# Kernel optimization log

Measured on AMD Instinct MI355X. Metric: run time of the kernel, lower is better.

Reference implementation:

```python
import jax, jax.numpy as jnp
import numpy as np

H = 8          # num_heads
DM = 128       # dmodel
BN_EPS = 1e-5


def _linear(x, w, b):
    # w stored as [in, out]
    return x @ w + b


def _relu_mha(q, k, v, qw, qb, kw, kb, vw, vb, ow, ob, mask):
    """TemMulHeadAtte: ReLU on projected Q/K/V, masked softmax, ReLU out-proj.
    q,k: [B,N,T,2*DM]; v: [B,N,T,DM]; mask: broadcastable to [B,N,H,T,T] or None."""
    B, N, T, _ = q.shape
    Q = jax.nn.relu(_linear(q, qw, qb)).reshape(B, N, T, H, -1)  # e = 2*DM/H
    K = jax.nn.relu(_linear(k, kw, kb)).reshape(B, N, T, H, -1)
    V = jax.nn.relu(_linear(v, vw, vb)).reshape(B, N, T, H, -1)  # d = DM/H
    scale = 1.0 / np.sqrt(Q.shape[-1]).astype(np.float32)
    scores = jnp.einsum('bnthe,bnshe->bnhts', Q, K)
    if mask is not None:
        scores = jnp.where(mask, -jnp.inf, scores)
    attn = jax.nn.softmax(scale * scores, axis=-1)  # dropout p=0 -> identity
    out = jnp.einsum('bnhts,bnshd->bnthd', attn, V).reshape(B, N, T, -1)
    return jax.nn.relu(_linear(out, ow, ob))


def setup_inputs() -> dict:
    key = jax.random.key(0)
    ks = iter(jax.random.split(key, 32))
    B, N, T = 16, 207, 24
    def w(shape, scale=0.05):
        return (jax.random.normal(next(ks), shape, dtype=jnp.float32) * scale)
    inp = {
        'x': w((B, N, T, DM), 1.0),
        'hidden': w((B, N, T, DM), 1.0),
        'tXin': w((B, N, T, DM), 1.0),
    }
    dk = 2 * DM // H * H   # 256
    dv = DM // H * H       # 128
    for pre in ('s', 't'):  # space / temporal attention params
        inp[pre + 'q_w'] = w((2 * DM, dk)); inp[pre + 'q_b'] = w((dk,))
        inp[pre + 'k_w'] = w((2 * DM, dk)); inp[pre + 'k_b'] = w((dk,))
        inp[pre + 'v_w'] = w((DM, dv));     inp[pre + 'v_b'] = w((dv,))
        inp[pre + 'o_w'] = w((dv, DM));     inp[pre + 'o_b'] = w((DM,))
    inp['gate_w'] = w((2 * DM, DM)); inp['gate_b'] = w((DM,))
    inp['bn_gamma'] = jnp.ones((DM,), jnp.float32)
    inp['bn_beta'] = jnp.zeros((DM,), jnp.float32)
    return inp


def reference(x, hidden, tXin,
              sq_w, sq_b, sk_w, sk_b, sv_w, sv_b, so_w, so_b,
              tq_w, tq_b, tk_w, tk_b, tv_w, tv_b, to_w, to_b,
              gate_w, gate_b, bn_gamma, bn_beta):
    B, N, T, E = hidden.shape
    ht = jnp.concatenate([hidden, tXin], axis=3)  # [B,N,T,2*DM]
    # spatial attention: attend over nodes (N<->T permute)
    sqk = ht.transpose(0, 2, 1, 3)        # [B,T,N,2*DM]
    sval = hidden.transpose(0, 2, 1, 3)   # [B,T,N,DM]
    spaceOut = _relu_mha(sqk, sqk, sval, sq_w, sq_b, sk_w, sk_b, sv_w, sv_b,
                         so_w, so_b, None).transpose(0, 2, 1, 3)  # [B,N,T,DM]
    # temporal attention with causal (strict upper-tri) mask
    mask = jnp.triu(jnp.ones((T, T), dtype=bool), 1)[None, None, None]
    tempOut = _relu_mha(ht, ht, hidden, tq_w, tq_b, tk_w, tk_b, tv_w, tv_b,
                        to_w, to_b, mask)  # [B,N,T,DM]
    # gate + BatchNorm2d over channel dim (training-mode batch stats, biased var)
    gi = _linear(jnp.concatenate([spaceOut, tempOut], axis=3), gate_w, gate_b)
    mean = gi.mean(axis=(0, 1, 2))
    var = gi.var(axis=(0, 1, 2))
    z = jax.nn.sigmoid((gi - mean) * jax.lax.rsqrt(var + BN_EPS) * bn_gamma + bn_beta)
    return z * spaceOut + (1.0 - z) * tempOut
```

## Files before the change

kernel.cpp:

```cpp
#include <hip/hip_runtime.h>
#include <hip/hip_bf16.h>

typedef __bf16 bf16;
typedef __bf16 bf16x2 __attribute__((ext_vector_type(2)));
typedef __bf16 bf16x8 __attribute__((ext_vector_type(8)));
typedef float f32x4 __attribute__((ext_vector_type(4)));

#define MTOT 79488
#define NDIM 207
#define TDIM 24

#define EXP2F(x) __builtin_amdgcn_exp2f(x)

__global__ void detect_dtype(const void* __restrict__ hidden, int* __restrict__ flag,
                             float* __restrict__ stats)
{
    __shared__ int cnt;
    if (threadIdx.x == 0) cnt = 0;
    stats[threadIdx.x] = 0.f;
    __syncthreads();
    const bf16* h = (const bf16*)hidden;
    int local = 0;
    for (int i = threadIdx.x; i < 4096; i += 256) {
        float v = (float)h[i];
        if (!(fabsf(v) < 1e6f)) local++;
    }
    atomicAdd(&cnt, local);
    __syncthreads();
    if (threadIdx.x == 0) *flag = (cnt > 8) ? 1 : 0;
}

__device__ inline float ld_ext(const void* p, int idx, int isF32)
{
    return isF32 ? ((const float*)p)[idx] : (float)((const bf16*)p)[idx];
}

__global__ __launch_bounds__(256) void prep_weights(
    const void* __restrict__ sq, const void* __restrict__ sk, const void* __restrict__ sv,
    const void* __restrict__ so, const void* __restrict__ tq, const void* __restrict__ tk,
    const void* __restrict__ tv, const void* __restrict__ to_, const void* __restrict__ gw,
    const void* __restrict__ sqb, const void* __restrict__ skb, const void* __restrict__ svb,
    const void* __restrict__ sob, const void* __restrict__ tqb, const void* __restrict__ tkb,
    const void* __restrict__ tvb, const void* __restrict__ tob, const void* __restrict__ gb,
    bf16* __restrict__ wdst, bf16* __restrict__ bdst, const int* __restrict__ dtf)
{
    const int isF32 = *dtf;
    if (blockIdx.x == 1536) {
        for (int j = threadIdx.x; j < 1664; j += 256) {
            const void* src; int i2;
            if      (j < 256)  { src = sqb; i2 = j; }
            else if (j < 512)  { src = skb; i2 = j - 256; }
            else if (j < 640)  { src = svb; i2 = j - 512; }
            else if (j < 896)  { src = tqb; i2 = j - 640; }
            else if (j < 1152) { src = tkb; i2 = j - 896; }
            else if (j < 1280) { src = tvb; i2 = j - 1152; }
            else if (j < 1408) { src = sob; i2 = j - 1280; }
            else if (j < 1536) { src = tob; i2 = j - 1408; }
            else               { src = gb;  i2 = j - 1536; }
            bdst[j] = (bf16)ld_ext(src, i2, isF32);
        }
        return;
    }
    const int e = blockIdx.x * 256 + threadIdx.x;
    float v;
    if (e < 327680) {
        int br = (e >= 163840);
        int e2 = e - br * 163840;
        int n = e2 >> 8, k = e2 & 255;
        const void* qw = br ? tq : sq;
        const void* kw = br ? tk : sk;
        const void* vw = br ? tv : sv;
        if      (n < 256) v = ld_ext(qw, k * 256 + n, isF32);
        else if (n < 512) v = ld_ext(kw, k * 256 + (n - 256), isF32);
        else              v = (k < 128) ? ld_ext(vw, k * 128 + (n - 512), isF32) : 0.f;
    } else if (e < 360448) {
        int br = (e >= 344064);
        int e2 = e - 327680 - br * 16384;
        int n = e2 >> 7, k = e2 & 127;
        v = ld_ext(br ? to_ : so, k * 128 + n, isF32);
    } else {
        int e2 = e - 360448;
        int n = e2 >> 8, k = e2 & 255;
        v = ld_ext(gw, k * 128 + n, isF32);
    }
    wdst[e] = (bf16)v;
}

__global__ __launch_bounds__(256) void gemm_bt(
    const void* __restrict__ A0v, const void* __restrict__ A1v,
    const void* __restrict__ A0bv,
    const bf16* __restrict__ Bt, const bf16* __restrict__ bias,
    bf16* __restrict__ Ca, bf16* __restrict__ Cb,
    int Nout, int Ktot, int doRelu, int aExt,
    const int* __restrict__ dtf, int pmA, int pmB,
    float* __restrict__ stats, int ntx, int nSplit, int mSplit)
{
    const int aF32 = aExt & *dtf;
    __shared__ bf16 smem[2 * 128 * 72];
    bf16* As = smem;
    bf16* Bs = smem + 128 * 72;
    __shared__ float lsum[128], lsq[128];
    const int tid  = threadIdx.x;
    const int wid  = tid >> 6, lane = tid & 63;
    const int wm   = (wid >> 1) * 64, wn = (wid & 1) * 64;
    const int quad = lane >> 4, l16 = lane & 15;

    int panel, n0;
    {
        const int nwg = (int)gridDim.x;
        const int lid = (int)blockIdx.x;
        const int q = nwg >> 3, r = nwg & 7;
        const int xcd = lid & 7, idx = lid >> 3;
        const int nid = (xcd < r ? xcd * (q + 1) : r * (q + 1) + (xcd - r) * q) + idx;
        panel = nid / ntx;
        n0 = (nid % ntx) * 128;
    }
    const int gB = (panel >= mSplit);
    if (gB) panel -= mSplit;
    const int m0 = panel * 128;
    const int brOff = gB ? Nout : 0;

    const int lrow = tid >> 3;
    const int lcol = (tid & 7) * 8;

    bf16x8 av[4], bv[4];
    auto loadTiles = [&](int k0) {
        const void* Ap = gB ? A0bv : ((k0 < 128) ? A0v : A1v);
        const int koff = (k0 < 128) ? k0 : k0 - 128;
        #pragma unroll
        for (int p = 0; p < 4; ++p) {
            int r = lrow + p * 32;
            if (aF32) {
                const float* Af = (const float*)Ap;
                f32x4 lo = *(const f32x4*)(Af + (size_t)(m0 + r) * 128 + koff + lcol);
                f32x4 hi = *(const f32x4*)(Af + (size_t)(m0 + r) * 128 + koff + lcol + 4);
                bf16x8 t;
                t[0]=(bf16)lo[0]; t[1]=(bf16)lo[1]; t[2]=(bf16)lo[2]; t[3]=(bf16)lo[3];
                t[4]=(bf16)hi[0]; t[5]=(bf16)hi[1]; t[6]=(bf16)hi[2]; t[7]=(bf16)hi[3];
                av[p] = t;
            } else {
                av[p] = *(const bf16x8*)((const bf16*)Ap + (size_t)(m0 + r) * 128 + koff + lcol);
            }
            bv[p] = *(const bf16x8*)(Bt + (size_t)(n0 + brOff + r) * Ktot + k0 + lcol);
        }
    };

    loadTiles(0);
    f32x4 acc[4][4] = {};

    for (int k0 = 0; k0 < Ktot; k0 += 64) {
        #pragma unroll
        for (int p = 0; p < 4; ++p) {
            int r = lrow + p * 32;
            *(bf16x8*)&As[r * 72 + lcol] = av[p];
            *(bf16x8*)&Bs[r * 72 + lcol] = bv[p];
        }
        __syncthreads();
        if (k0 + 64 < Ktot) loadTiles(k0 + 64);
        #pragma unroll
        for (int kk = 0; kk < 64; kk += 32) {
            bf16x8 af[4], bfr[4];
            #pragma unroll
            for (int i = 0; i < 4; ++i)
                af[i] = *(const bf16x8*)&As[(wm + i * 16 + l16) * 72 + kk + quad * 8];
            #pragma unroll
            for (int j = 0; j < 4; ++j)
                bfr[j] = *(const bf16x8*)&Bs[(wn + j * 16 + l16) * 72 + kk + quad * 8];
            #pragma unroll
            for (int i = 0; i < 4; ++i)
                #pragma unroll
                for (int j = 0; j < 4; ++j)
                    acc[i][j] = __builtin_amdgcn_mfma_f32_16x16x32_bf16(
                        af[i], bfr[j], acc[i][j], 0, 0, 0);
        }
        __syncthreads();
    }

    bf16* Cp; int pm; int c0;
    if (nSplit && n0 >= nSplit) { Cp = Cb; pm = pmB; c0 = n0 - nSplit; }
    else if (gB)                { Cp = Cb; pm = pmB; c0 = n0; }
    else                        { Cp = Ca; pm = pmA; c0 = n0; }

    if (stats) {
        if (tid < 128) { lsum[tid] = 0.f; lsq[tid] = 0.f; }
        __syncthreads();
    }
    #pragma unroll
    for (int j = 0; j < 4; ++j) {
        int col = n0 + brOff + wn + j * 16 + l16;
        float bv2 = (float)bias[col];
        float ps = 0.f, psq = 0.f;
        #pragma unroll
        for (int i = 0; i < 4; ++i) {
            #pragma unroll
            for (int r = 0; r < 4; ++r) {
                float v = acc[i][j][r] + bv2;
                if (doRelu) v = fmaxf(v, 0.f);
                if (stats) { ps += v; psq += v * v; }
                acc[i][j][r] = v;
            }
        }
        if (stats) {
            atomicAdd(&lsum[col & 127], ps);
            atomicAdd(&lsq[col & 127], psq);
        }
    }

    bf16* Cs = smem;
    #pragma unroll
    for (int j = 0; j < 4; ++j)
        #pragma unroll
        for (int i = 0; i < 4; ++i)
            #pragma unroll
            for (int r = 0; r < 4; ++r)
                Cs[(wm + i * 16 + quad * 4 + r) * 132 + wn + j * 16 + l16]
                    = (bf16)acc[i][j][r];
    __syncthreads();

    if (stats && tid < 128) {
        atomicAdd(&stats[tid], lsum[tid]);
        atomicAdd(&stats[128 + tid], lsq[tid]);
    }

    const int srow = tid >> 4, scol = (tid & 15) * 8;
    #pragma unroll
    for (int pass = 0; pass < 8; ++pass) {
        int rl = pass * 16 + srow;
        int m = m0 + rl;
        int o;
        if (pm == 1) {
            int t = m % 24, bn = m / 24;
            int n = bn % 207, b = bn / 207;
            o = (b * 24 + t) * 207 + n;
        } else if (pm == 2) {
            int n = m % 207, bt = m / 207;
            int t = bt % 24, b = bt / 24;
            o = (b * 207 + n) * 24 + t;
        } else {
            o = m;
        }
        bf16x8 v = *(const bf16x8*)&Cs[rl * 132 + scol];
        *(bf16x8*)&Cp[(size_t)o * Nout + c0 + scol] = v;
    }
}

__device__ inline int kpos(int i)
{
    return (i < 16) ? (i << 1) : (((i - 16) << 1) | 1);
}

__global__ __launch_bounds__(256) void attn_spatial_mfma(
    const bf16* __restrict__ QKV, bf16* __restrict__ O)
{
    const int hh = blockIdx.x, t = blockIdx.y, b = blockIdx.z;
    __shared__ bf16 Ks[208 * 40];
    __shared__ bf16 Vt[16 * 232];
    __shared__ bf16 Pl[4][2][16 * 40];
    const int tid = threadIdx.x;
    const int wave = tid >> 6, lane = tid & 63;
    const int quad = lane >> 4, l16 = lane & 15;
    const size_t R = (size_t)(b * TDIM + t) * NDIM;

    for (int idx = tid; idx < 832; idx += 256) {
        int n = idx >> 2, seg = (idx & 3) * 8;
        bf16x8 v8 = {};
        if (n < NDIM)
            v8 = *(const bf16x8*)(QKV + (R + n) * 640 + 256 + hh * 32 + seg);
        *(bf16x8*)&Ks[n * 40 + seg] = v8;
    }
    for (int idx = tid; idx < 448; idx += 256) {
        int s = idx >> 1, half = (idx & 1) * 8;
        bf16x8 v8 = {};
        if (s < NDIM)
            v8 = *(const bf16x8*)(QKV + (R + s) * 640 + 512 + hh * 16 + half);
        int spos = (s & ~31) + kpos(s & 31);
        #pragma unroll
        for (int j = 0; j < 8; ++j)
            Vt[(half + j) * 232 + spos] = v8[j];
    }
    __syncthreads();

    const float k2 = 0.25506538410868237f;

    for (int qt = wave; qt < 13; qt += 4) {
        const int q0 = qt * 16;
        int qrow = q0 + l16; if (qrow >= NDIM) qrow = NDIM - 1;
        bf16x8 qfrag = *(const bf16x8*)(QKV + (R + qrow) * 640 + hh * 32 + quad * 8);
        f32x4 s[13];
        #pragma unroll
        for (int c = 0; c < 13; ++c) {
            bf16x8 kf = *(const bf16x8*)&Ks[(c * 16 + l16) * 40 + quad * 8];
            f32x4 z = {};
            s[c] = __builtin_amdgcn_mfma_f32_16x16x32_bf16(qfrag, kf, z, 0, 0, 0);
        }
        float linv[4];
        #pragma unroll
        for (int r = 0; r < 4; ++r) {
            float sum = 0.f;
            #pragma unroll
            for (int c = 0; c < 13; ++c) {
                float p = EXP2F(s[c][r] * k2);
                if (c == 12 && l16 == 15) p = 0.f;
                s[c][r] = p;
                sum += p;
            }
            sum += __shfl_xor(sum, 1);
            sum += __shfl_xor(sum, 2);
            sum += __shfl_xor(sum, 4);
            sum += __shfl_xor(sum, 8);
            linv[r] = __builtin_amdgcn_rcpf(sum);
        }
        f32x4 oacc = {};
        #pragma unroll
        for (int sc = 0; sc < 7; ++sc) {
            bf16* pb = &Pl[wave][sc & 1][0];
            #pragma unroll
            for (int r = 0; r < 4; ++r) {
                bf16x2 pk;
                pk[0] = (bf16)s[2 * sc][r];
                pk[1] = (sc < 6) ? (bf16)s[2 * sc + 1][r] : (bf16)0.f;
                *(bf16x2*)&pb[(quad * 4 + r) * 40 + 2 * l16] = pk;
            }
            bf16x8 pf = *(const bf16x8*)&pb[l16 * 40 + quad * 8];
            bf16x8 vf = *(const bf16x8*)&Vt[l16 * 232 + sc * 32 + quad * 8];
            oacc = __builtin_amdgcn_mfma_f32_16x16x32_bf16(pf, vf, oacc, 0, 0, 0);
        }
        #pragma unroll
        for (int r = 0; r < 4; ++r) {
            int row = q0 + quad * 4 + r;
            if (row < NDIM)
                O[(R + row) * 128 + hh * 16 + l16] = (bf16)(oacc[r] * linv[r]);
        }
    }
}

__global__ __launch_bounds__(256) void attn_temporal_mfma(
    const bf16* __restrict__ QKV, bf16* __restrict__ O)
{
    const size_t m0 = (size_t)blockIdx.x * TDIM;
    __shared__ bf16 Khs[8 * 32 * 40];
    __shared__ bf16 Vts[8 * 16 * 40];
    __shared__ bf16 Pl[4][2][16 * 40];
    const int tid = threadIdx.x;
    const int wave = tid >> 6, lane = tid & 63;
    const int quad = lane >> 4, l16 = lane & 15;
    const int STR = 640;

    for (int idx = tid; idx < 32 * 32; idx += 256) {
        int row = idx >> 5, seg = idx & 31;
        int h = seg >> 2, j = (seg & 3) * 8;
        bf16x8 v8 = {};
        if (row < TDIM)
            v8 = *(const bf16x8*)(QKV + (m0 + row) * STR + 256 + h * 32 + j);
        *(bf16x8*)&Khs[h * 1280 + row * 40 + j] = v8;
    }
    for (int idx = tid; idx < 32 * 128; idx += 256) {
        int s = idx >> 7, c = idx & 127;
        int h = c >> 4, d = c & 15;
        bf16 v = (bf16)0.f;
        if (s < TDIM) v = QKV[(m0 + s) * STR + 512 + h * 16 + d];
        Vts[h * 640 + d * 40 + kpos(s)] = v;
    }
    __syncthreads();

    const float k2 = 0.25506538410868237f;

    #pragma unroll
    for (int hi = 0; hi < 2; ++hi) {
        const int h = wave * 2 + hi;
        #pragma unroll
        for (int qt = 0; qt < 2; ++qt) {
            int qrow = qt * 16 + l16; if (qrow >= TDIM) qrow = TDIM - 1;
            bf16x8 qfrag = *(const bf16x8*)(QKV + (m0 + qrow) * STR + h * 32 + quad * 8);
            bf16x8 kf0 = *(const bf16x8*)&Khs[h * 1280 + l16 * 40 + quad * 8];
            bf16x8 kf1 = *(const bf16x8*)&Khs[h * 1280 + (16 + l16) * 40 + quad * 8];
            f32x4 z = {};
            f32x4 s0 = __builtin_amdgcn_mfma_f32_16x16x32_bf16(qfrag, kf0, z, 0, 0, 0);
            f32x4 s1 = __builtin_amdgcn_mfma_f32_16x16x32_bf16(qfrag, kf1, z, 0, 0, 0);
            bf16* pb = &Pl[wave][qt][0];
            float linv[4];
            #pragma unroll
            for (int r = 0; r < 4; ++r) {
                int q = qt * 16 + quad * 4 + r;
                float p0 = (l16 <= q)      ? EXP2F(s0[r] * k2) : 0.f;
                float p1 = (16 + l16 <= q) ? EXP2F(s1[r] * k2) : 0.f;
                float sum = p0 + p1;
                sum += __shfl_xor(sum, 1);
                sum += __shfl_xor(sum, 2);
                sum += __shfl_xor(sum, 4);
                sum += __shfl_xor(sum, 8);
                linv[r] = __builtin_amdgcn_rcpf(sum);
                bf16x2 pk; pk[0] = (bf16)p0; pk[1] = (bf16)p1;
                *(bf16x2*)&pb[(quad * 4 + r) * 40 + 2 * l16] = pk;
            }
            bf16x8 pf = *(const bf16x8*)&pb[l16 * 40 + quad * 8];
            bf16x8 vf = *(const bf16x8*)&Vts[h * 640 + l16 * 40 + quad * 8];
            f32x4 oacc = __builtin_amdgcn_mfma_f32_16x16x32_bf16(pf, vf, z, 0, 0, 0);
            #pragma unroll
            for (int r = 0; r < 4; ++r) {
                int row = qt * 16 + quad * 4 + r;
                if (row < TDIM)
                    O[(m0 + row) * 128 + h * 16 + l16] = (bf16)(oacc[r] * linv[r]);
            }
        }
    }
}

__global__ __launch_bounds__(256) void bn_final(
    const bf16* __restrict__ gi, const bf16* __restrict__ sp, const bf16* __restrict__ tp,
    const void* __restrict__ gammav, const void* __restrict__ betav,
    const float* __restrict__ stats, void* __restrict__ outv,
    const int* __restrict__ dtf)
{
    const int isF32 = *dtf;
    const size_t base = ((size_t)blockIdx.x * 256 + threadIdx.x) * 8;
    const int c0 = (int)(base & 127);
    const float invM = 1.f / (float)MTOT;
    bf16x8 g8 = *(const bf16x8*)(gi + base);
    bf16x8 s8 = *(const bf16x8*)(sp + base);
    bf16x8 t8 = *(const bf16x8*)(tp + base);
    float res[8];
    #pragma unroll
    for (int j = 0; j < 8; ++j) {
        int c = c0 + j;
        float mean = stats[c] * invM;
        float var  = stats[128 + c] * invM - mean * mean;
        float gam = ld_ext(gammav, c, isF32);
        float bet = ld_ext(betav, c, isF32);
        float g = (float)g8[j];
        float zn = (g - mean) * rsqrtf(var + 1e-5f) * gam + bet;
        float z = 1.f / (1.f + EXP2F(zn * -1.4426950408889634f));
        float sv = (float)s8[j], tv = (float)t8[j];
        res[j] = z * sv + (1.f - z) * tv;
    }
    if (isF32) {
        float* op = (float*)outv + base;
        f32x4 lo = {res[0], res[1], res[2], res[3]};
        f32x4 hi = {res[4], res[5], res[6], res[7]};
        *(f32x4*)op = lo;
        *(f32x4*)(op + 4) = hi;
    } else {
        bf16x8 o8;
        #pragma unroll
        for (int j = 0; j < 8; ++j) o8[j] = (bf16)res[j];
        *(bf16x8*)((bf16*)outv + base) = o8;
    }
}

extern "C" void kernel_launch(void* const* d_in, const int* in_sizes, int n_in,
                              void* d_out, int out_size, void* d_ws, size_t ws_size,
                              hipStream_t stream)
{
    const void* hidden = d_in[1];
    const void* tXin   = d_in[2];
    const void* sq_w = d_in[3];  const void* sq_b = d_in[4];
    const void* sk_w = d_in[5];  const void* sk_b = d_in[6];
    const void* sv_w = d_in[7];  const void* sv_b = d_in[8];
    const void* so_w = d_in[9];  const void* so_b = d_in[10];
    const void* tq_w = d_in[11]; const void* tq_b = d_in[12];
    const void* tk_w = d_in[13]; const void* tk_b = d_in[14];
    const void* tv_w = d_in[15]; const void* tv_b = d_in[16];
    const void* to_w = d_in[17]; const void* to_b = d_in[18];
    const void* gate_w = d_in[19]; const void* gate_b = d_in[20];
    const void* gamma  = d_in[21]; const void* beta   = d_in[22];

    char* ws = (char*)d_ws;
    float* stats = (float*)ws;
    int*  dtf    = (int*)(ws + 1024);
    bf16* bB     = (bf16*)(ws + 2048);
    bf16* wT     = (bf16*)(ws + 8192);
    bf16* spaceO = (bf16*)(ws + 794624);
    bf16* attnOs = (bf16*)(ws + 21143552);
    bf16* QKVs   = (bf16*)(ws + 41492480);
    bf16* attnOt = (bf16*)(ws + 143237120);
    bf16* QKVt   = (bf16*)(ws + 163586048);
    bf16* gi     = QKVs;

    const int tier = (ws_size >= 265330688ull) ? 2
                   : (ws_size >= 163586048ull) ? 1 : 0;
    if (tier == 0) attnOt = attnOs;
    bf16* tempO = attnOt;
    bf16* sW  = wT;            bf16* tW  = wT + 163840;
    bf16* soT = wT + 327680;
    bf16* gwT = wT + 360448;
    const int BIG = 1 << 28;

    detect_dtype<<<1, 256, 0, stream>>>(hidden, dtf, stats);
    prep_weights<<<dim3(1537), 256, 0, stream>>>(
        sq_w, sk_w, sv_w, so_w, tq_w, tk_w, tv_w, to_w, gate_w,
        sq_b, sk_b, sv_b, so_b, tq_b, tk_b, tv_b, to_b, gate_b,
        wT, bB, dtf);

    if (tier == 2) {
        gemm_bt<<<dim3(6210), 256, 0, stream>>>(
            hidden, tXin, nullptr, wT, bB, QKVs, QKVt,
            640, 256, 1, 1, dtf, 1, 0, nullptr, 10, 640, BIG);
        attn_spatial_mfma<<<dim3(8, TDIM, 16), 256, 0, stream>>>(QKVs, attnOs);
        attn_temporal_mfma<<<dim3(16 * NDIM), 256, 0, stream>>>(QKVt, attnOt);
    } else {
        gemm_bt<<<dim3(3105), 256, 0, stream>>>(
            hidden, tXin, nullptr, sW, bB, QKVs, nullptr,
            640, 256, 1, 1, dtf, 1, 0, nullptr, 5, 0, BIG);
        attn_spatial_mfma<<<dim3(8, TDIM, 16), 256, 0, stream>>>(QKVs, attnOs);
        if (tier == 0) {
            gemm_bt<<<dim3(621), 256, 0, stream>>>(
                attnOs, nullptr, nullptr, soT, bB + 1280, spaceO, nullptr,
                128, 128, 1, 0, dtf, 2, 0, nullptr, 1, 0, BIG);
        }
        gemm_bt<<<dim3(3105), 256, 0, stream>>>(
            hidden, tXin, nullptr, tW, bB + 640, QKVs, nullptr,
            640, 256, 1, 1, dtf, 0, 0, nullptr, 5, 0, BIG);
        attn_temporal_mfma<<<dim3(16 * NDIM), 256, 0, stream>>>(QKVs, attnOt);
    }

    if (tier >= 1) {
        gemm_bt<<<dim3(1242), 256, 0, stream>>>(
            attnOs, nullptr, attnOt, soT, bB + 1280, spaceO, tempO,
            128, 128, 1, 0, dtf, 2, 0, nullptr, 1, 0, 621);
    } else {
        gemm_bt<<<dim3(621), 256, 0, stream>>>(
            attnOt, nullptr, nullptr, soT + 16384, bB + 1408, tempO, nullptr,
            128, 128, 1, 0, dtf, 0, 0, nullptr, 1, 0, BIG);
    }

    gemm_bt<<<dim3(621), 256, 0, stream>>>(
        spaceO, tempO, nullptr, gwT, bB + 1536, gi, nullptr,
        128, 256, 0, 0, dtf, 0, 0, stats, 1, 0, BIG);
    bn_final<<<dim3(4968), 256, 0, stream>>>(gi, spaceO, tempO, gamma, beta, stats, d_out, dtf);
}
```

Measured before the change: 543.1 us.

## Pre-convert inputs to bf16 and split fused QKV GEMM into sequential passes

Adds a kernel that converts hidden and tXin to bf16 buffers once, so the two QKV projection GEMMs read bf16 instead of converting fp32 on every tile load. The single combined spatial+temporal QKV GEMM (6210 blocks writing two outputs) becomes two separate GEMM+attention passes that reuse one QKV buffer. Attention P scratch drops from double to single buffering. This frees workspace and lowers A-operand traffic, but adds an extra conversion pass and serialises the two QKV GEMMs.

```diff
diff --git a/kernel.cpp b/kernel.cpp
--- a/kernel.cpp
+++ b/kernel.cpp
@@ -33,6 +33,26 @@
 __device__ inline float ld_ext(const void* p, int idx, int isF32)
 {
     return isF32 ? ((const float*)p)[idx] : (float)((const bf16*)p)[idx];
+}
+
+__global__ __launch_bounds__(256) void cvt_inputs(
+    const void* __restrict__ hidden, const void* __restrict__ tXin,
+    bf16* __restrict__ hb, bf16* __restrict__ tb, const int* __restrict__ dtf)
+{
+    const int isF32 = *dtf;
+    const void* src = blockIdx.y ? tXin : hidden;
+    bf16* dst = blockIdx.y ? tb : hb;
+    const size_t e8 = ((size_t)blockIdx.x * 256 + threadIdx.x) * 8;
+    bf16x8 v;
+    if (isF32) {
+        f32x4 lo = *(const f32x4*)((const float*)src + e8);
+        f32x4 hi = *(const f32x4*)((const float*)src + e8 + 4);
+        v[0]=(bf16)lo[0]; v[1]=(bf16)lo[1]; v[2]=(bf16)lo[2]; v[3]=(bf16)lo[3];
+        v[4]=(bf16)hi[0]; v[5]=(bf16)hi[1]; v[6]=(bf16)hi[2]; v[7]=(bf16)hi[3];
+    } else {
+        v = *(const bf16x8*)((const bf16*)src + e8);
+    }
+    *(bf16x8*)(dst + e8) = v;
 }
 
 __global__ __launch_bounds__(256) void prep_weights(
@@ -93,7 +113,7 @@
     bf16* __restrict__ Ca, bf16* __restrict__ Cb,
     int Nout, int Ktot, int doRelu, int aExt,
     const int* __restrict__ dtf, int pmA, int pmB,
-    float* __restrict__ stats, int ntx, int nSplit, int mSplit)
+    float* __restrict__ stats, int ntx, int mSplit)
 {
     const int aF32 = aExt & *dtf;
     __shared__ bf16 smem[2 * 128 * 72];
@@ -176,10 +196,8 @@
         __syncthreads();
     }
 
-    bf16* Cp; int pm; int c0;
-    if (nSplit && n0 >= nSplit) { Cp = Cb; pm = pmB; c0 = n0 - nSplit; }
-    else if (gB)                { Cp = Cb; pm = pmB; c0 = n0; }
-    else                        { Cp = Ca; pm = pmA; c0 = n0; }
+    bf16* Cp = gB ? Cb : Ca;
+    const int pm = gB ? pmB : pmA;
 
     if (stats) {
         if (tid < 128) { lsum[tid] = 0.f; lsq[tid] = 0.f; }
@@ -240,7 +258,7 @@
             o = m;
         }
         bf16x8 v = *(const bf16x8*)&Cs[rl * 132 + scol];
-        *(bf16x8*)&Cp[(size_t)o * Nout + c0 + scol] = v;
+        *(bf16x8*)&Cp[(size_t)o * Nout + n0 + scol] = v;
     }
 }
 
@@ -255,7 +273,7 @@
     const int hh = blockIdx.x, t = blockIdx.y, b = blockIdx.z;
     __shared__ bf16 Ks[208 * 40];
     __shared__ bf16 Vt[16 * 232];
-    __shared__ bf16 Pl[4][2][16 * 40];
+    __shared__ bf16 Pl[4][16 * 40];
     const int tid = threadIdx.x;
     const int wave = tid >> 6, lane = tid & 63;
     const int quad = lane >> 4, l16 = lane & 15;
@@ -311,9 +329,9 @@
             linv[r] = __builtin_amdgcn_rcpf(sum);
         }
         f32x4 oacc = {};
+        bf16* pb = &Pl[wave][0];
         #pragma unroll
         for (int sc = 0; sc < 7; ++sc) {
-            bf16* pb = &Pl[wave][sc & 1][0];
             #pragma unroll
             for (int r = 0; r < 4; ++r) {
                 bf16x2 pk;
@@ -340,7 +358,7 @@
     const size_t m0 = (size_t)blockIdx.x * TDIM;
     __shared__ bf16 Khs[8 * 32 * 40];
     __shared__ bf16 Vts[8 * 16 * 40];
-    __shared__ bf16 Pl[4][2][16 * 40];
+    __shared__ bf16 Pl[4][16 * 40];
     const int tid = threadIdx.x;
     const int wave = tid >> 6, lane = tid & 63;
     const int quad = lane >> 4, l16 = lane & 15;
@@ -377,7 +395,7 @@
             f32x4 z = {};
             f32x4 s0 = __builtin_amdgcn_mfma_f32_16x16x32_bf16(qfrag, kf0, z, 0, 0, 0);
             f32x4 s1 = __builtin_amdgcn_mfma_f32_16x16x32_bf16(qfrag, kf1, z, 0, 0, 0);
-            bf16* pb = &Pl[wave][qt][0];
+            bf16* pb = &Pl[wave][0];
             float linv[4];
             #pragma unroll
             for (int r = 0; r < 4; ++r) {
@@ -472,16 +490,17 @@
     bf16* spaceO = (bf16*)(ws + 794624);
     bf16* attnOs = (bf16*)(ws + 21143552);
     bf16* QKVs   = (bf16*)(ws + 41492480);
-    bf16* attnOt = (bf16*)(ws + 143237120);
-    bf16* QKVt   = (bf16*)(ws + 163586048);
+    bf16* hb     = (bf16*)(ws + 143237120);
+    bf16* tb     = (bf16*)(ws + 163586048);
+    bf16* attnOt = (bf16*)(ws + 183934976);
     bf16* gi     = QKVs;
 
-    const int tier = (ws_size >= 265330688ull) ? 2
-                   : (ws_size >= 163586048ull) ? 1 : 0;
-    if (tier == 0) attnOt = attnOs;
+    const int tier = (ws_size >= 204283904ull) ? 2
+                   : (ws_size >= 183934976ull) ? 1 : 0;
+    if (tier < 2) attnOt = attnOs;
     bf16* tempO = attnOt;
     bf16* sW  = wT;            bf16* tW  = wT + 163840;
-    bf16* soT = wT + 327680;
+    bf16* soT = wT + 327680;   bf16* toT = wT + 344064;
     bf16* gwT = wT + 360448;
     const int BIG = 1 << 28;
 
@@ -490,41 +509,40 @@
         sq_w, sk_w, sv_w, so_w, tq_w, tk_w, tv_w, to_w, gate_w,
         sq_b, sk_b, sv_b, so_b, tq_b, tk_b, tv_b, to_b, gate_b,
         wT, bB, dtf);
-
-    if (tier == 2) {
-        gemm_bt<<<dim3(6210), 256, 0, stream>>>(
-            hidden, tXin, nullptr, wT, bB, QKVs, QKVt,
-            640, 256, 1, 1, dtf, 1, 0, nullptr, 10, 640, BIG);
-        attn_spatial_mfma<<<dim3(8, TDIM, 16), 256, 0, stream>>>(QKVs, attnOs);
-        attn_temporal_mfma<<<dim3(16 * NDIM), 256, 0, stream>>>(QKVt, attnOt);
-    } else {
-        gemm_bt<<<dim3(3105), 256, 0, stream>>>(
-            hidden, tXin, nullptr, sW, bB, QKVs, nullptr,
-            640, 256, 1, 1, dtf, 1, 0, nullptr, 5, 0, BIG);
-        attn_spatial_mfma<<<dim3(8, TDIM, 16), 256, 0, stream>>>(QKVs, attnOs);
-        if (tier == 0) {
-            gemm_bt<<<dim3(621), 256, 0, stream>>>(
-                attnOs, nullptr, nullptr, soT, bB + 1280, spaceO, nullptr,
-                128, 128, 1, 0, dtf, 2, 0, nullptr, 1, 0, BIG);
-        }
-        gemm_bt<<<dim3(3105), 256, 0, stream>>>(
-            hidden, tXin, nullptr, tW, bB + 640, QKVs, nullptr,
-            640, 256, 1, 1, dtf, 0, 0, nullptr, 5, 0, BIG);
-        attn_temporal_mfma<<<dim3(16 * NDIM), 256, 0, stream>>>(QKVs, attnOt);
-    }
-
-    if (tier >= 1) {
+    if (tier >= 1)
+        cvt_inputs<<<dim3(4968, 2), 256, 0, stream>>>(hidden, tXin, hb, tb, dtf);
+
+    const void* A0 = (tier >= 1) ? (const void*)hb : hidden;
+    const void* A1 = (tier >= 1) ? (const void*)tb : tXin;
+    const int aExt = (tier >= 1) ? 0 : 1;
+
+    gemm_bt<<<dim3(3105), 256, 0, stream>>>(
+        A0, A1, nullptr, sW, bB, QKVs, nullptr,
+        640, 256, 1, aExt, dtf, 1, 0, nullptr, 5, BIG);
+    attn_spatial_mfma<<<dim3(8, TDIM, 16), 256, 0, stream>>>(QKVs, attnOs);
+    if (tier < 2) {
+        gemm_bt<<<dim3(621), 256, 0, stream>>>(
+            attnOs, nullptr, nullptr, soT, bB + 1280, spaceO, nullptr,
+            128, 128, 1, 0, dtf, 2, 0, nullptr, 1, BIG);
+    }
+
+    gemm_bt<<<dim3(3105), 256, 0, stream>>>(
+        A0, A1, nullptr, tW, bB + 640, QKVs, nullptr,
+        640, 256, 1, aExt, dtf, 0, 0, nullptr, 5, BIG);
+    attn_temporal_mfma<<<dim3(16 * NDIM), 256, 0, stream>>>(QKVs, attnOt);
+
+    if (tier >= 2) {
         gemm_bt<<<dim3(1242), 256, 0, stream>>>(
             attnOs, nullptr, attnOt, soT, bB + 1280, spaceO, tempO,
-            128, 128, 1, 0, dtf, 2, 0, nullptr, 1, 0, 621);
+            128, 128, 1, 0, dtf, 2, 0, nullptr, 1, 621);
     } else {
         gemm_bt<<<dim3(621), 256, 0, stream>>>(
-            attnOt, nullptr, nullptr, soT + 16384, bB + 1408, tempO, nullptr,
-            128, 128, 1, 0, dtf, 0, 0, nullptr, 1, 0, BIG);
+            attnOt, nullptr, nullptr, toT, bB + 1408, tempO, nullptr,
+            128, 128, 1, 0, dtf, 0, 0, nullptr, 1, BIG);
     }
 
     gemm_bt<<<dim3(621), 256, 0, stream>>>(
         spaceO, tempO, nullptr, gwT, bB + 1536, gi, nullptr,
-        128, 256, 0, 0, dtf, 0, 0, stats, 1, 0, BIG);
+        128, 256, 0, 0, dtf, 0, 0, stats, 1, BIG);
     bn_final<<<dim3(4968), 256, 0, stream>>>(gi, spaceO, tempO, gamma, beta, stats, d_out, dtf);
 }
```

Measured after the change: 497.3 us. 8.4% less time.
